# Optimization experiments

Hardware: AMD Instinct MI355X
Metric: run time of the kernel (lower is better)

Reference implementation:

```python
import jax, jax.numpy as jnp
import numpy as np

N = 50000
E = 400000
R = 6
DIMS = (20, 256, 256, 512)


def setup_inputs() -> dict:
    key = jax.random.key(0)
    ks = jax.random.split(key, 16)
    inp = {
        "x": jax.random.normal(ks[0], (N, DIMS[0]), dtype=jnp.float32),
        "edge_index": jax.random.randint(ks[1], (2, E), 0, N, dtype=jnp.int64),
        "edge_type": jax.random.randint(ks[2], (E,), 0, R, dtype=jnp.int64),
    }
    # RGCN layer params: relation weights [R, in, out], root weight [in, out], bias [out]
    for li, (din, dout) in enumerate(zip(DIMS, DIMS[1:])):
        s = 1.0 / np.sqrt(din)
        inp[f"W{li}"] = jax.random.normal(ks[3 + 3 * li], (R, din, dout), dtype=jnp.float32) * s
        inp[f"root{li}"] = jax.random.normal(ks[4 + 3 * li], (din, dout), dtype=jnp.float32) * s
        inp[f"b{li}"] = jnp.zeros((dout,), dtype=jnp.float32)
    return inp


def _rgcn_layer(x, src, dst, etype, W, root, b):
    # Relation-specific transform of all nodes: [R, N, dout]
    h = jnp.einsum('ni,rio->rno', x, W)
    # Gather per-edge messages h[etype[e], src[e]] -> [E, dout]
    msgs = h[etype, src]
    # Mean-aggregate per (destination, relation) segment (PyG aggr='mean')
    seg = dst * R + etype  # [E]
    sums = jax.ops.segment_sum(msgs, seg, num_segments=N * R)          # [N*R, dout]
    cnt = jax.ops.segment_sum(jnp.ones((msgs.shape[0],), x.dtype), seg, num_segments=N * R)
    mean = sums / jnp.maximum(cnt, 1.0)[:, None]
    agg = mean.reshape(N, R, -1).sum(axis=1)  # sum over relations
    return agg + x @ root + b


def reference(x, edge_index, edge_type, W0, root0, b0, W1, root1, b1, W2, root2, b2):
    src, dst = edge_index[0], edge_index[1]  # messages flow source -> target
    params = ((W0, root0, b0), (W1, root1, b1), (W2, root2, b2))
    h = x
    for (W, root, b) in params:
        h = _rgcn_layer(h, src, dst, edge_type, W, root, b)
        h = jax.nn.relu(h)
    h = jnp.tanh(h)
    z = jnp.max(h, axis=0)          # graph-level max pool over nodes -> [latent]
    z = z / jnp.linalg.norm(z)      # normalized latent space
    return z[None, :]               # [1, latent]
```

## Files before the change

### kernel.cpp

```cpp
#include <hip/hip_runtime.h>

#define N_NODES 50000
#define N_EDGES 400000
#define N_REL 6
#define NSEG (N_NODES * N_REL)
#define NTILE ((N_NODES + 63) / 64)

#define SCAN_TILE 1024
#define SCAN_NB ((NSEG + SCAN_TILE - 1) / SCAN_TILE)

typedef float4 f4;
typedef short bf16x8 __attribute__((ext_vector_type(8)));
typedef float f32x4 __attribute__((ext_vector_type(4)));
typedef float f32x16 __attribute__((ext_vector_type(16)));
typedef int i32x8 __attribute__((ext_vector_type(8)));
typedef int i32x4 __attribute__((ext_vector_type(4)));

__device__ __forceinline__ unsigned enc_f32(float f) {
    unsigned u = __float_as_uint(f);
    return (u & 0x80000000u) ? ~u : (u | 0x80000000u);
}
__device__ __forceinline__ float dec_f32(unsigned e) {
    return __uint_as_float((e & 0x80000000u) ? (e ^ 0x80000000u) : ~e);
}
__device__ __forceinline__ unsigned short bf16_rne(float x) {
    unsigned u = __float_as_uint(x);
    return (unsigned short)((u + 0x7FFFu + ((u >> 16) & 1u)) >> 16);
}
__device__ __forceinline__ unsigned fp8x4(float a0, float a1, float a2, float a3) {
    unsigned r = __builtin_amdgcn_cvt_pk_fp8_f32(a0, a1, 0, 0);
    r = __builtin_amdgcn_cvt_pk_fp8_f32(a2, a3, r, 1);
    return r;
}
__device__ __forceinline__ unsigned char fp8_1(float v) {
    return (unsigned char)(__builtin_amdgcn_cvt_pk_fp8_f32(v, v, 0, 0) & 0xFF);
}

#define SWZ(row, slot) ((size_t)(row) * 32 + (((slot) ^ (((row) >> 1) & 3)) * 8))

__global__ void count_seg(const int* __restrict__ ei, const int* __restrict__ et,
                          int* __restrict__ cnt) {
    int e = blockIdx.x * blockDim.x + threadIdx.x;
    if (e < N_EDGES) atomicAdd(&cnt[ei[N_EDGES + e] * N_REL + et[e]], 1);
}

__global__ void scan1(int* __restrict__ cnt, int* __restrict__ bsum) {
    __shared__ int sh[256];
    int t = threadIdx.x, b = blockIdx.x;
    int base = b * SCAN_TILE + t * 4;
    int v[4]; int s = 0;
    #pragma unroll
    for (int i = 0; i < 4; ++i) {
        v[i] = (base + i < NSEG) ? cnt[base + i] : 0;
        s += v[i];
    }
    sh[t] = s; __syncthreads();
    for (int o = 1; o < 256; o <<= 1) {
        int x = (t >= o) ? sh[t - o] : 0;
        __syncthreads();
        sh[t] += x;
        __syncthreads();
    }
    int run = sh[t] - s;
    #pragma unroll
    for (int i = 0; i < 4; ++i) {
        if (base + i < NSEG) cnt[base + i] = run;
        run += v[i];
    }
    if (t == 255) bsum[b] = sh[255];
}

__global__ void scan2(int* __restrict__ bsum) {
    __shared__ int sh[512];
    int t = threadIdx.x;
    int v = (t < SCAN_NB) ? bsum[t] : 0;
    sh[t] = v; __syncthreads();
    for (int o = 1; o < 512; o <<= 1) {
        int x = (t >= o) ? sh[t - o] : 0;
        __syncthreads();
        sh[t] += x;
        __syncthreads();
    }
    if (t < SCAN_NB) bsum[t] = sh[t] - v;
}

__global__ void scan3(const int* __restrict__ part, const int* __restrict__ bsum,
                      int* __restrict__ rowptr, int* __restrict__ fillptr) {
    int t = threadIdx.x, b = blockIdx.x;
    int base = b * SCAN_TILE + t * 4;
    int off = bsum[b];
    #pragma unroll
    for (int i = 0; i < 4; ++i) {
        if (base + i < NSEG) {
            int v = part[base + i] + off;
            rowptr[base + i] = v;
            fillptr[base + i] = v;
        }
    }
    if (b == 0 && t == 0) rowptr[NSEG] = N_EDGES;
}

__global__ void fill_edges(const int* __restrict__ ei, const int* __restrict__ et,
                           int* __restrict__ fillptr, int* __restrict__ esrc) {
    int e = blockIdx.x * blockDim.x + threadIdx.x;
    if (e < N_EDGES) {
        int seg = ei[N_EDGES + e] * N_REL + et[e];
        int p = atomicAdd(&fillptr[seg], 1);
        esrc[p] = ei[e];
    }
}

__global__ void rcp_kernel(const int* __restrict__ rowptr, float* __restrict__ rcp) {
    int s = blockIdx.x * blockDim.x + threadIdx.x;
    if (s < NSEG) {
        int c = rowptr[s + 1] - rowptr[s];
        rcp[s] = 1.0f / (float)(c > 1 ? c : 1);
    }
}

__global__ void prep_w0(const float* __restrict__ Wf, const float* __restrict__ rootW,
                        unsigned short* __restrict__ Wt,
                        int K1, int din, int dout, int KB) {
    int k = blockIdx.x;
    int n = blockIdx.y * 256 + threadIdx.x;
    if (n >= dout) return;
    float v = 0.f;
    if (k < K1) v = Wf[(size_t)k * dout + n];
    else if (k < K1 + din) v = rootW[(size_t)(k - K1) * dout + n];
    Wt[(size_t)n * KB + k] = bf16_rne(v);
}

__global__ void prep_wpk8(const float* __restrict__ Wf, const float* __restrict__ rootW,
                          unsigned char* __restrict__ Wpk, int K1, int dout) {
    int k = blockIdx.x;
    int ct = blockIdx.y;
    int nl = threadIdx.x;
    int col = ct * 256 + nl;
    float v = (k < K1) ? Wf[(size_t)k * dout + col]
                       : rootW[(size_t)(k - K1) * dout + col];
    v *= 16.0f;
    int p = k >> 6;
    Wpk[((size_t)(ct * 28 + p)) * 16384 + (size_t)nl * 64 + (k & 63)] = fp8_1(v);
}

__global__ void gather0(const float* __restrict__ x, const int* __restrict__ rowptr,
                        const int* __restrict__ esrc, const float* __restrict__ rcp,
                        unsigned short* __restrict__ Abf0) {
    int idx = blockIdx.x * blockDim.x + threadIdx.x;
    if (idx >= NSEG * 5) return;
    int s = idx / 5, q = idx - s * 5;
    float ax = 0.f, ay = 0.f, az = 0.f, aw = 0.f;
    int e0 = rowptr[s], e1 = rowptr[s + 1];
    for (int e = e0; e < e1; ++e) {
        const f4 u = *(const f4*)&x[(size_t)esrc[e] * 20 + q * 4];
        ax += u.x; ay += u.y; az += u.z; aw += u.w;
    }
    float sc = rcp[s];
    int node = s / N_REL, rel = s - node * N_REL;
    unsigned short* p = &Abf0[(size_t)node * 160 + rel * 20 + q * 4];
    unsigned o0 = bf16_rne(ax * sc) | ((unsigned)bf16_rne(ay * sc) << 16);
    unsigned o1 = bf16_rne(az * sc) | ((unsigned)bf16_rne(aw * sc) << 16);
    *(unsigned*)(p + 0) = o0;
    *(unsigned*)(p + 2) = o1;
}

__global__ void copyx0(const float* __restrict__ x, unsigned short* __restrict__ Abf0) {
    int t = blockIdx.x * blockDim.x + threadIdx.x;
    int n = t >> 5, d = t & 31;
    if (n >= N_NODES || d >= 20) return;
    Abf0[(size_t)n * 160 + 120 + d] = bf16_rne(x[(size_t)n * 20 + d]);
}

__global__ void gather_all8(const unsigned char* __restrict__ h8, const int* __restrict__ rowptr,
                            const int* __restrict__ esrc, const float* __restrict__ rcp,
                            unsigned char* __restrict__ Apk) {
    int t = blockIdx.x * blockDim.x + threadIdx.x;
    int sl = t >> 3;
    int q = t & 7;
    if (sl < NSEG) {
        int e0 = rowptr[sl], e1 = rowptr[sl + 1];
        float a[32];
        #pragma unroll
        for (int i = 0; i < 32; ++i) a[i] = 0.f;
        for (int e = e0; e < e1; ++e) {
            const unsigned char* hp = &h8[(size_t)esrc[e] * 256 + q * 32];
            #pragma unroll
            for (int c = 0; c < 2; ++c) {
                int4 v = *(const int4*)&hp[c * 16];
                const unsigned* pu = (const unsigned*)&v;
                #pragma unroll
                for (int j = 0; j < 4; ++j) {
                    unsigned u = pu[j];
                    a[c * 16 + j * 4 + 0] += __builtin_amdgcn_cvt_f32_fp8(u, 0);
                    a[c * 16 + j * 4 + 1] += __builtin_amdgcn_cvt_f32_fp8(u, 1);
                    a[c * 16 + j * 4 + 2] += __builtin_amdgcn_cvt_f32_fp8(u, 2);
                    a[c * 16 + j * 4 + 3] += __builtin_amdgcn_cvt_f32_fp8(u, 3);
                }
            }
        }
        float sc = rcp[sl];
        int node = sl / 6, rel = sl - node * 6;
        int rt = node >> 6, m = node & 63;
        int ks = rel * 8 + q;
        unsigned ow[8];
        #pragma unroll
        for (int i = 0; i < 8; ++i)
            ow[i] = fp8x4(a[4 * i] * sc, a[4 * i + 1] * sc, a[4 * i + 2] * sc, a[4 * i + 3] * sc);
        int p = ks >> 1, sp = ks & 1;
        unsigned char* dst = Apk + ((size_t)(rt * 28 + p)) * 4096 + (size_t)m * 64;
        int rot = (m >> 1) & 3;
        *(int4*)(dst + (((sp * 2 + 0 + rot) & 3) * 16)) = make_int4(ow[0], ow[1], ow[2], ow[3]);
        *(int4*)(dst + (((sp * 2 + 1 + rot) & 3) * 16)) = make_int4(ow[4], ow[5], ow[6], ow[7]);
    } else if (sl < NSEG + N_NODES) {
        int node = sl - NSEG;
        int rt = node >> 6, m = node & 63;
        const unsigned char* hp = &h8[(size_t)node * 256 + q * 32];
        int4 lo = *(const int4*)(hp + 0);
        int4 hi = *(const int4*)(hp + 16);
        int ks = 48 + q;
        int p = ks >> 1, sp = ks & 1;
        unsigned char* dst = Apk + ((size_t)(rt * 28 + p)) * 4096 + (size_t)m * 64;
        int rot = (m >> 1) & 3;
        *(int4*)(dst + (((sp * 2 + 0 + rot) & 3) * 16)) = lo;
        *(int4*)(dst + (((sp * 2 + 1 + rot) & 3) * 16)) = hi;
    }
}

__global__ __launch_bounds__(256)
void gemm_l0(const unsigned short* __restrict__ A, const unsigned short* __restrict__ Wt,
             const float* __restrict__ bias, unsigned char* __restrict__ outH8,
             int Ktot, int KB, int dout) {
    __shared__ unsigned short As[64 * 32];
    __shared__ unsigned short Bs[256 * 32];
    const int tid = threadIdx.x;
    const int col0 = blockIdx.x * 256;
    const int row0 = blockIdx.y * 64;
    const int w = tid >> 6, l = tid & 63;
    f32x4 acc[4][4] = {};

    for (int k0 = 0; k0 < Ktot; k0 += 32) {
        {
            int m = tid >> 2, slot = tid & 3;
            int4 v = {0, 0, 0, 0};
            int mg = row0 + m;
            if (mg < N_NODES) v = *(const int4*)&A[(size_t)mg * Ktot + k0 + slot * 8];
            *(int4*)&As[SWZ(m, slot)] = v;
        }
        {
            int nb = tid >> 2, slot = tid & 3;
            #pragma unroll
            for (int j = 0; j < 4; ++j) {
                int n = nb + j * 64;
                int4 v = *(const int4*)&Wt[(size_t)(col0 + n) * KB + k0 + slot * 8];
                *(int4*)&Bs[SWZ(n, slot)] = v;
            }
        }
        __syncthreads();
        bf16x8 af[4], bfr[4];
        #pragma unroll
        for (int rf = 0; rf < 4; ++rf)
            af[rf] = *(const bf16x8*)&As[SWZ(rf * 16 + (l & 15), l >> 4)];
        #pragma unroll
        for (int cf = 0; cf < 4; ++cf)
            bfr[cf] = *(const bf16x8*)&Bs[SWZ(w * 64 + cf * 16 + (l & 15), l >> 4)];
        #pragma unroll
        for (int cf = 0; cf < 4; ++cf)
            #pragma unroll
            for (int rf = 0; rf < 4; ++rf)
                acc[rf][cf] = __builtin_amdgcn_mfma_f32_16x16x32_bf16(
                    af[rf], bfr[cf], acc[rf][cf], 0, 0, 0);
        __syncthreads();
    }

    const int colbase = col0 + w * 64;
    #pragma unroll
    for (int cf = 0; cf < 4; ++cf) {
        int c = colbase + cf * 16 + (l & 15);
        float bb = bias[c];
        #pragma unroll
        for (int rf = 0; rf < 4; ++rf)
            #pragma unroll
            for (int i = 0; i < 4; ++i) {
                int m = row0 + rf * 16 + (l >> 4) * 4 + i;
                if (m < N_NODES) {
                    float v = fmaxf(acc[rf][cf][i] + bb, 0.f);
                    outH8[(size_t)m * dout + c] = fp8_1(v);
                }
            }
    }
}

__global__ __launch_bounds__(256)
void gemm_mx(const unsigned char* __restrict__ Apk, const unsigned char* __restrict__ Wpk,
             const float* __restrict__ bias, unsigned char* __restrict__ outH8,
             unsigned* __restrict__ maxbuf, int dout, int fuse) {
    __shared__ unsigned lmax[256];

    const int tid = threadIdx.x;
    const int w = tid >> 6, l = tid & 63;
    int by, bx;
    if (fuse) {
        int hw = blockIdx.x;
        if (hw < 1552) { by = ((hw >> 4) << 3) | (hw & 7); bx = (hw >> 3) & 1; }
        else { int r = hw - 1552; by = 776 + (r % 6); bx = r / 6; }
    } else {
        by = blockIdx.x; bx = 0;
    }
    const int row0 = by * 64;
    const int bcol = bx * 256;
    const int cg0 = bcol + w * 64;
    const int ctIdx = cg0 >> 8;
    const int nOff = cg0 & 255;

    const unsigned char* aT = Apk + (size_t)by * 28 * 4096;
    const unsigned char* bLane = Wpk + (size_t)ctIdx * 28 * 16384
                               + (size_t)(nOff + (l & 31)) * 64 + (size_t)(l >> 5) * 32;
    const int rot = (l >> 1) & 3;
    const int g = (l >> 5) * 2;
    const int o00 = (l & 31) * 64 + (((g + 0 + rot) & 3) * 16);
    const int o01 = (l & 31) * 64 + (((g + 1 + rot) & 3) * 16);
    const int o10 = o00 + 2048;
    const int o11 = o01 + 2048;

    f32x16 acc[2][2] = {};
    i32x4 A0[3], A1[3], A2[3], A3[3];
    i32x4 B0[3], B1[3], B2[3], B3[3];

#define SB() __builtin_amdgcn_sched_barrier(0)

#define LOADP(p, s) do {                                                     \
        const unsigned char* _ap = aT + (size_t)(p) * 4096;                  \
        const unsigned char* _bp = bLane + (size_t)(p) * 16384;              \
        asm volatile("global_load_dwordx4 %0, %1, off"                       \
                     : "=&v"(A0[s]) : "v"(_ap + o00));                       \
        asm volatile("global_load_dwordx4 %0, %1, off"                       \
                     : "=&v"(A1[s]) : "v"(_ap + o01));                       \
        asm volatile("global_load_dwordx4 %0, %1, off"                       \
                     : "=&v"(A2[s]) : "v"(_ap + o10));                       \
        asm volatile("global_load_dwordx4 %0, %1, off"                       \
                     : "=&v"(A3[s]) : "v"(_ap + o11));                       \
        asm volatile("global_load_dwordx4 %0, %1, off"                       \
                     : "=&v"(B0[s]) : "v"(_bp));                             \
        asm volatile("global_load_dwordx4 %0, %1, off offset:16"             \
                     : "=&v"(B1[s]) : "v"(_bp));                             \
        asm volatile("global_load_dwordx4 %0, %1, off offset:2048"           \
                     : "=&v"(B2[s]) : "v"(_bp));                             \
        asm volatile("global_load_dwordx4 %0, %1, off offset:2064"           \
                     : "=&v"(B3[s]) : "v"(_bp));                             \
    } while (0)

#define DOP(s) do {                                                          \
        i32x8 a0 = __builtin_shufflevector(A0[s], A1[s], 0,1,2,3,4,5,6,7);   \
        i32x8 a1 = __builtin_shufflevector(A2[s], A3[s], 0,1,2,3,4,5,6,7);   \
        i32x8 b0 = __builtin_shufflevector(B0[s], B1[s], 0,1,2,3,4,5,6,7);   \
        i32x8 b1 = __builtin_shufflevector(B2[s], B3[s], 0,1,2,3,4,5,6,7);   \
        acc[0][0] = __builtin_amdgcn_mfma_scale_f32_32x32x64_f8f6f4(         \
            a0, b0, acc[0][0], 0, 0, 0, 127, 0, 123);                        \
        acc[1][0] = __builtin_amdgcn_mfma_scale_f32_32x32x64_f8f6f4(         \
            a1, b0, acc[1][0], 0, 0, 0, 127, 0, 123);                        \
        acc[0][1] = __builtin_amdgcn_mfma_scale_f32_32x32x64_f8f6f4(         \
            a0, b1, acc[0][1], 0, 0, 0, 127, 0, 123);                        \
        acc[1][1] = __builtin_amdgcn_mfma_scale_f32_32x32x64_f8f6f4(         \
            a1, b1, acc[1][1], 0, 0, 0, 127, 0, 123);                        \
    } while (0)

#define STEP(p, WN) do {                                                     \
        asm volatile("s_waitcnt vmcnt(" WN ")");                             \
        SB();                                                                \
        __builtin_amdgcn_s_setprio(1);                                       \
        DOP((p) % 3);                                                        \
        __builtin_amdgcn_s_setprio(0);                                       \
        SB();                                                                \
        if ((p) + 3 < 28) LOADP((p) + 3, (p) % 3);                           \
        SB();                                                                \
    } while (0)

    LOADP(0, 0);
    LOADP(1, 1);
    LOADP(2, 2);
    SB();

    STEP(0,  "16"); STEP(1,  "16"); STEP(2,  "16"); STEP(3,  "16");
    STEP(4,  "16"); STEP(5,  "16"); STEP(6,  "16"); STEP(7,  "16");
    STEP(8,  "16"); STEP(9,  "16"); STEP(10, "16"); STEP(11, "16");
    STEP(12, "16"); STEP(13, "16"); STEP(14, "16"); STEP(15, "16");
    STEP(16, "16"); STEP(17, "16"); STEP(18, "16"); STEP(19, "16");
    STEP(20, "16"); STEP(21, "16"); STEP(22, "16"); STEP(23, "16");
    STEP(24, "16"); STEP(25, "16"); STEP(26, "8");  STEP(27, "0");

    asm volatile("s_waitcnt vmcnt(0)");
    SB();

#undef STEP
#undef DOP
#undef LOADP
#undef SB

    if (!fuse) {
        #pragma unroll
        for (int cf = 0; cf < 2; ++cf) {
            int c = cg0 + cf * 32 + (l & 31);
            float bb = bias[c];
            #pragma unroll
            for (int rf = 0; rf < 2; ++rf)
                #pragma unroll
                for (int reg = 0; reg < 16; ++reg) {
                    int m = row0 + rf * 32 + (reg & 3) + 8 * (reg >> 2) + 4 * (l >> 5);
                    if (m < N_NODES) {
                        float v = fmaxf(acc[rf][cf][reg] + bb, 0.f);
                        outH8[(size_t)m * dout + c] = fp8_1(v);
                    }
                }
        }
    } else {
        lmax[tid] = 0u;
        __syncthreads();
        #pragma unroll
        for (int cf = 0; cf < 2; ++cf) {
            int c = cg0 + cf * 32 + (l & 31);
            float bb = bias[c];
            float mv = 0.f;
            bool any = false;
            #pragma unroll
            for (int rf = 0; rf < 2; ++rf)
                #pragma unroll
                for (int reg = 0; reg < 16; ++reg) {
                    int m = row0 + rf * 32 + (reg & 3) + 8 * (reg >> 2) + 4 * (l >> 5);
                    if (m < N_NODES) {
                        float v = acc[rf][cf][reg] + bb;
                        mv = any ? fmaxf(mv, v) : v;
                        any = true;
                    }
                }
            if (any) atomicMax(&lmax[c - bcol], enc_f32(mv));
        }
        __syncthreads();
        atomicMax(&maxbuf[bcol + tid], lmax[tid]);
    }
}

__global__ void finalize_kernel(const unsigned* __restrict__ maxbuf,
                                float* __restrict__ out) {
    __shared__ float red[8];
    int c = threadIdx.x;
    float v = dec_f32(maxbuf[c]);
    v = fmaxf(v, 0.0f);
    float t = tanhf(v);
    float s = t * t;
    #pragma unroll
    for (int o = 32; o > 0; o >>= 1) s += __shfl_down(s, o);
    int wid = c >> 6;
    if ((c & 63) == 0) red[wid] = s;
    __syncthreads();
    if (c < 8) {
        float wsum = red[c];
        #pragma unroll
        for (int o = 4; o > 0; o >>= 1) wsum += __shfl_down(wsum, o);
        if (c == 0) red[0] = wsum;
    }
    __syncthreads();
    float norm = sqrtf(red[0]);
    out[c] = t / norm;
}

static inline size_t align_up(size_t v, size_t a) { return (v + a - 1) / a * a; }

extern "C" void kernel_launch(void* const* d_in, const int* in_sizes, int n_in,
                              void* d_out, int out_size, void* d_ws, size_t ws_size,
                              hipStream_t stream) {
    const float* x  = (const float*)d_in[0];
    const int*   ei = (const int*)d_in[1];
    const int*   et = (const int*)d_in[2];
    const float* W0 = (const float*)d_in[3];
    const float* r0 = (const float*)d_in[4];
    const float* b0 = (const float*)d_in[5];
    const float* W1 = (const float*)d_in[6];
    const float* r1 = (const float*)d_in[7];
    const float* b1 = (const float*)d_in[8];
    const float* W2 = (const float*)d_in[9];
    const float* r2 = (const float*)d_in[10];
    const float* b2 = (const float*)d_in[11];
    float* out = (float*)d_out;

    char* ws = (char*)d_ws;
    size_t off = 0;
    int* cntpart = (int*)(ws + off); off = align_up(off + (size_t)NSEG * 4, 256);
    int* bsum = (int*)(ws + off);    off = align_up(off + 512 * 4, 256);
    int* rowptr = (int*)(ws + off);  off = align_up(off + (size_t)(NSEG + 1) * 4, 256);
    int* fillptr = (int*)(ws + off); off = align_up(off + (size_t)NSEG * 4, 256);
    int* esrc = (int*)(ws + off);    off = align_up(off + (size_t)N_EDGES * 4, 256);
    float* rcp = (float*)(ws + off); off = align_up(off + (size_t)NSEG * 4, 256);
    unsigned* maxbuf = (unsigned*)(ws + off); off = align_up(off + 512 * 4, 256);
    unsigned short* Wt0 = (unsigned short*)(ws + off); off = align_up(off + (size_t)256 * 160 * 2, 256);
    unsigned char* Wpk1 = (unsigned char*)(ws + off); off = align_up(off + (size_t)1 * 28 * 16384, 256);
    unsigned char* Wpk2 = (unsigned char*)(ws + off); off = align_up(off + (size_t)2 * 28 * 16384, 256);
    unsigned char* hbuf1 = (unsigned char*)(ws + off); off = align_up(off + (size_t)N_NODES * 256, 256);
    unsigned char* hbuf2 = (unsigned char*)(ws + off); off = align_up(off + (size_t)N_NODES * 256, 256);
    unsigned short* Abf0 = (unsigned short*)(ws + off); off = align_up(off + (size_t)N_NODES * 160 * 2, 256);
    unsigned char* Apk = (unsigned char*)(ws + off); off = align_up(off + (size_t)NTILE * 28 * 4096, 256);
    if (ws_size < off) return;

    hipMemsetAsync(cntpart, 0, (size_t)NSEG * 4, stream);
    count_seg<<<(N_EDGES + 255) / 256, 256, 0, stream>>>(ei, et, cntpart);
    scan1<<<SCAN_NB, 256, 0, stream>>>(cntpart, bsum);
    scan2<<<1, 512, 0, stream>>>(bsum);
    scan3<<<SCAN_NB, 256, 0, stream>>>(cntpart, bsum, rowptr, fillptr);
    rcp_kernel<<<(NSEG + 255) / 256, 256, 0, stream>>>(rowptr, rcp);
    fill_edges<<<(N_EDGES + 255) / 256, 256, 0, stream>>>(ei, et, fillptr, esrc);
    hipMemsetAsync(maxbuf, 0, 512 * 4, stream);

    prep_w0<<<dim3(160, 1), 256, 0, stream>>>(W0, r0, Wt0, 120, 20, 256, 160);
    prep_wpk8<<<dim3(1792, 1), 256, 0, stream>>>(W1, r1, Wpk1, 1536, 256);
    prep_wpk8<<<dim3(1792, 2), 256, 0, stream>>>(W2, r2, Wpk2, 1536, 512);

    hipMemsetAsync(Abf0, 0, (size_t)N_NODES * 160 * 2, stream);
    gather0<<<(NSEG * 5 + 255) / 256, 256, 0, stream>>>(x, rowptr, esrc, rcp, Abf0);
    copyx0<<<(N_NODES * 32 + 255) / 256, 256, 0, stream>>>(x, Abf0);
    gemm_l0<<<dim3(1, NTILE), 256, 0, stream>>>(Abf0, Wt0, b0, hbuf1, 160, 160, 256);

    const int gthreads = (NSEG + N_NODES) * 8;

    gather_all8<<<(gthreads + 255) / 256, 256, 0, stream>>>(hbuf1, rowptr, esrc, rcp, Apk);
    gemm_mx<<<dim3(NTILE), 256, 0, stream>>>(Apk, Wpk1, b1, hbuf2, nullptr, 256, 0);

    gather_all8<<<(gthreads + 255) / 256, 256, 0, stream>>>(hbuf2, rowptr, esrc, rcp, Apk);
    gemm_mx<<<dim3(2 * NTILE), 256, 0, stream>>>(Apk, Wpk2, b2, nullptr, maxbuf, 512, 1);

    finalize_kernel<<<1, 512, 0, stream>>>(maxbuf, out);
}
```

Baseline: 321.2 us.

## Repack FP8 A/B tiles into lane-contiguous fragment layout for coalesced MFMA loads

Changes the packed FP8 layout of both the activation tiles (written by the gather kernel) and the weight tiles (written by prep_wpk8) so each MFMA fragment is stored as 64 lanes × 16 bytes contiguously. The GEMM then issues global loads with a single per-lane base plus fixed immediate offsets. This replaces the rotated, strided 64-byte-row accesses with fully contiguous 1 KB wavefront loads. The cost is scattered 16-byte writes in the packing kernels and a layout that all three kernels must keep in sync.

```diff
diff --git a/kernel.cpp b/kernel.cpp
--- a/kernel.cpp
+++ b/kernel.cpp
@@ -139,8 +139,13 @@
     float v = (k < K1) ? Wf[(size_t)k * dout + col]
                        : rootW[(size_t)(k - K1) * dout + col];
     v *= 16.0f;
-    int p = k >> 6;
-    Wpk[((size_t)(ct * 28 + p)) * 16384 + (size_t)nl * 64 + (k & 63)] = fp8_1(v);
+    int c = nl & 63, wv = nl >> 6;
+    int p = k >> 6, kl = k & 63;
+    int half = kl >> 5, klo = kl & 31;
+    int j = ((c >> 5) << 1) + (klo >> 4);
+    int l = (half << 5) + (c & 31);
+    Wpk[(((size_t)(ct * 28 + p)) * 4 + wv) * 4096
+        + (size_t)j * 1024 + (size_t)l * 16 + (klo & 15)] = fp8_1(v);
 }
 
 __global__ void gather0(const float* __restrict__ x, const int* __restrict__ rowptr,
@@ -206,11 +211,12 @@
         #pragma unroll
         for (int i = 0; i < 8; ++i)
             ow[i] = fp8x4(a[4 * i] * sc, a[4 * i + 1] * sc, a[4 * i + 2] * sc, a[4 * i + 3] * sc);
-        int p = ks >> 1, sp = ks & 1;
-        unsigned char* dst = Apk + ((size_t)(rt * 28 + p)) * 4096 + (size_t)m * 64;
-        int rot = (m >> 1) & 3;
-        *(int4*)(dst + (((sp * 2 + 0 + rot) & 3) * 16)) = make_int4(ow[0], ow[1], ow[2], ow[3]);
-        *(int4*)(dst + (((sp * 2 + 1 + rot) & 3) * 16)) = make_int4(ow[4], ow[5], ow[6], ow[7]);
+        int p = ks >> 1;
+        int l = ((ks & 1) << 5) + (m & 31);
+        unsigned char* dst = Apk + ((size_t)(rt * 28 + p)) * 4096
+                           + (size_t)((m >> 5) << 1) * 1024 + (size_t)l * 16;
+        *(int4*)(dst)        = make_int4(ow[0], ow[1], ow[2], ow[3]);
+        *(int4*)(dst + 1024) = make_int4(ow[4], ow[5], ow[6], ow[7]);
     } else if (sl < NSEG + N_NODES) {
         int node = sl - NSEG;
         int rt = node >> 6, m = node & 63;
@@ -218,11 +224,12 @@
         int4 lo = *(const int4*)(hp + 0);
         int4 hi = *(const int4*)(hp + 16);
         int ks = 48 + q;
-        int p = ks >> 1, sp = ks & 1;
-        unsigned char* dst = Apk + ((size_t)(rt * 28 + p)) * 4096 + (size_t)m * 64;
-        int rot = (m >> 1) & 3;
-        *(int4*)(dst + (((sp * 2 + 0 + rot) & 3) * 16)) = lo;
-        *(int4*)(dst + (((sp * 2 + 1 + rot) & 3) * 16)) = hi;
+        int p = ks >> 1;
+        int l = ((ks & 1) << 5) + (m & 31);
+        unsigned char* dst = Apk + ((size_t)(rt * 28 + p)) * 4096
+                           + (size_t)((m >> 5) << 1) * 1024 + (size_t)l * 16;
+        *(int4*)(dst)        = lo;
+        *(int4*)(dst + 1024) = hi;
     }
 }
 
@@ -310,17 +317,9 @@
     const int bcol = bx * 256;
     const int cg0 = bcol + w * 64;
     const int ctIdx = cg0 >> 8;
-    const int nOff = cg0 & 255;
-
-    const unsigned char* aT = Apk + (size_t)by * 28 * 4096;
-    const unsigned char* bLane = Wpk + (size_t)ctIdx * 28 * 16384
-                               + (size_t)(nOff + (l & 31)) * 64 + (size_t)(l >> 5) * 32;
-    const int rot = (l >> 1) & 3;
-    const int g = (l >> 5) * 2;
-    const int o00 = (l & 31) * 64 + (((g + 0 + rot) & 3) * 16);
-    const int o01 = (l & 31) * 64 + (((g + 1 + rot) & 3) * 16);
-    const int o10 = o00 + 2048;
-    const int o11 = o01 + 2048;
+
+    const unsigned char* aBase = Apk + (size_t)by * 28 * 4096 + (size_t)l * 16;
+    const unsigned char* bBase = Wpk + ((size_t)ctIdx * 28 * 4 + w) * 4096 + (size_t)l * 16;
 
     f32x16 acc[2][2] = {};
     i32x4 A0[3], A1[3], A2[3], A3[3];
@@ -329,23 +328,23 @@
 #define SB() __builtin_amdgcn_sched_barrier(0)
 
 #define LOADP(p, s) do {                                                     \
-        const unsigned char* _ap = aT + (size_t)(p) * 4096;                  \
-        const unsigned char* _bp = bLane + (size_t)(p) * 16384;              \
+        const unsigned char* _ap = aBase + (size_t)(p) * 4096;               \
+        const unsigned char* _bp = bBase + (size_t)(p) * 16384;              \
         asm volatile("global_load_dwordx4 %0, %1, off"                       \
-                     : "=&v"(A0[s]) : "v"(_ap + o00));                       \
-        asm volatile("global_load_dwordx4 %0, %1, off"                       \
-                     : "=&v"(A1[s]) : "v"(_ap + o01));                       \
-        asm volatile("global_load_dwordx4 %0, %1, off"                       \
-                     : "=&v"(A2[s]) : "v"(_ap + o10));                       \
-        asm volatile("global_load_dwordx4 %0, %1, off"                       \
-                     : "=&v"(A3[s]) : "v"(_ap + o11));                       \
+                     : "=&v"(A0[s]) : "v"(_ap));                             \
+        asm volatile("global_load_dwordx4 %0, %1, off offset:1024"           \
+                     : "=&v"(A1[s]) : "v"(_ap));                             \
+        asm volatile("global_load_dwordx4 %0, %1, off offset:2048"           \
+                     : "=&v"(A2[s]) : "v"(_ap));                             \
+        asm volatile("global_load_dwordx4 %0, %1, off offset:3072"           \
+                     : "=&v"(A3[s]) : "v"(_ap));                             \
         asm volatile("global_load_dwordx4 %0, %1, off"                       \
                      : "=&v"(B0[s]) : "v"(_bp));                             \
-        asm volatile("global_load_dwordx4 %0, %1, off offset:16"             \
+        asm volatile("global_load_dwordx4 %0, %1, off offset:1024"           \
                      : "=&v"(B1[s]) : "v"(_bp));                             \
         asm volatile("global_load_dwordx4 %0, %1, off offset:2048"           \
                      : "=&v"(B2[s]) : "v"(_bp));                             \
-        asm volatile("global_load_dwordx4 %0, %1, off offset:2064"           \
+        asm volatile("global_load_dwordx4 %0, %1, off offset:3072"           \
                      : "=&v"(B3[s]) : "v"(_bp));                             \
     } while (0)
 
```

Measured after the change: 311.2 us. -3.1%, faster.
